# Kernel optimization log

Hardware: AMD Instinct MI355X
Metric: run time of the kernel (lower is better)

Reference implementation:

```python
import jax, jax.numpy as jnp
import numpy as np

B, D_IN, D_DENSE, S1, S2 = 16384, 1024, 1024, 1024, 1024
SPARSITY1, SPARSITY2 = 0.1, 0.01  # fraction of zeros in the 'sparse' weights


def setup_inputs() -> dict:
    key = jax.random.key(0)
    kx, k0, k1, k2, km1, km2 = jax.random.split(key, 6)
    x = jax.random.normal(kx, (B, D_IN), dtype=jnp.float32)
    # dense layer params (nn.Linear): weight [out, in], bias [out]
    w0 = jax.random.normal(k0, (D_DENSE, D_IN), dtype=jnp.float32) / np.sqrt(D_IN)
    b0 = jnp.zeros((D_DENSE,), dtype=jnp.float32)
    # sparse layers: dense randn weight elementwise-masked (mask keeps with prob 1-sparsity)
    w1 = jax.random.normal(k1, (S1, D_DENSE), dtype=jnp.float32)
    mask1 = jax.random.uniform(km1, (S1, D_DENSE)) > SPARSITY1
    b1 = jnp.zeros((S1,), dtype=jnp.float32)
    w2 = jax.random.normal(k2, (S2, S1), dtype=jnp.float32)
    mask2 = jax.random.uniform(km2, (S2, S1)) > SPARSITY2
    b2 = jnp.zeros((S2,), dtype=jnp.float32)
    return {"x": x, "w0": w0, "b0": b0, "w1": w1, "b1": b1, "mask1": mask1,
            "w2": w2, "b2": b2, "mask2": mask2}


def reference(x, w0, b0, w1, b1, mask1, w2, b2, mask2):
    # layer 1: dense linear + ReLU
    h = jax.nn.relu(jnp.einsum('bi,oi->bo', x, w0) + b0)
    # layer 2: masked ('sparse' COO in torch) linear + bias + ReLU
    h = jax.nn.relu(jnp.einsum('bi,oi->bo', h, w1 * mask1) + b1)
    # layer 3: masked linear + bias + ReLU
    out = jax.nn.relu(jnp.einsum('bi,oi->bo', h, w2 * mask2) + b2)
    return out
```

## Files before the change

### kernel.cpp

```cpp
#include <hip/hip_runtime.h>
#include <hip/hip_bf16.h>
#include <cstdint>
#include <cstddef>


typedef __bf16 bf16x8 __attribute__((ext_vector_type(8)));
typedef float  f32x4  __attribute__((ext_vector_type(4)));

#define AS1 __attribute__((address_space(1)))
#define AS3 __attribute__((address_space(3)))

__device__ __forceinline__ void gload_lds16(const void* g, void* l) {
    __builtin_amdgcn_global_load_lds((const AS1 void*)g, (AS3 void*)l, 16, 0, 0);
}

__global__ void detect_mask(const unsigned char* __restrict__ m, int* __restrict__ flag) {
    if (threadIdx.x != 0 || blockIdx.x != 0) return;
    int or1 = 0, or3 = 0;
    for (int e = 0; e < 256; ++e) { or1 |= m[e * 4 + 1]; or3 |= m[e * 4 + 3]; }
    *flag = or1 ? 1 : (or3 ? 2 : 0);
}

__global__ void cvt_bf16(const float* __restrict__ in, __bf16* __restrict__ out, long n) {
    long i = ((long)blockIdx.x * blockDim.x + threadIdx.x) * 8;
    if (i >= n) return;
    float4 a = *reinterpret_cast<const float4*>(in + i);
    float4 b = *reinterpret_cast<const float4*>(in + i + 4);
    bf16x8 o;
    o[0] = (__bf16)a.x; o[1] = (__bf16)a.y; o[2] = (__bf16)a.z; o[3] = (__bf16)a.w;
    o[4] = (__bf16)b.x; o[5] = (__bf16)b.y; o[6] = (__bf16)b.z; o[7] = (__bf16)b.w;
    *reinterpret_cast<bf16x8*>(out + i) = o;
}

__global__ void prep_w(const float* __restrict__ w, const void* __restrict__ mask,
                       const int* __restrict__ flag, __bf16* __restrict__ out, long n) {
    long i = ((long)blockIdx.x * blockDim.x + threadIdx.x) * 8;
    if (i >= n) return;
    float4 a = *reinterpret_cast<const float4*>(w + i);
    float4 b = *reinterpret_cast<const float4*>(w + i + 4);
    float v[8] = {a.x, a.y, a.z, a.w, b.x, b.y, b.z, b.w};
    if (mask) {
        const int mode = *flag;
        if (mode == 1) {
            const unsigned char* mp = (const unsigned char*)mask;
            #pragma unroll
            for (int j = 0; j < 8; ++j) v[j] = mp[i + j] ? v[j] : 0.f;
        } else if (mode == 0) {
            const int* mp = (const int*)mask;
            #pragma unroll
            for (int j = 0; j < 8; ++j) v[j] = mp[i + j] ? v[j] : 0.f;
        } else {
            const float* mp = (const float*)mask;
            #pragma unroll
            for (int j = 0; j < 8; ++j) v[j] = (mp[i + j] != 0.f) ? v[j] : 0.f;
        }
    }
    bf16x8 o;
    #pragma unroll
    for (int j = 0; j < 8; ++j) o[j] = (__bf16)v[j];
    *reinterpret_cast<bf16x8*>(out + i) = o;
}

__device__ __forceinline__ f32x4 mfma16(bf16x8 a, bf16x8 b, f32x4 c) {
    return __builtin_amdgcn_mfma_f32_16x16x32_bf16(a, b, c, 0, 0, 0);
}

#define MFMAQ(Q, A00, A01, A10, A11)                                        \
    __builtin_amdgcn_s_setprio(1);                                          \
    _Pragma("unroll")                                                       \
    for (int n = 0; n < 4; ++n) {                                           \
        acc[2*(Q)][n]   = mfma16(A00, b[n][0], acc[2*(Q)][n]);              \
        acc[2*(Q)][n]   = mfma16(A01, b[n][1], acc[2*(Q)][n]);              \
        acc[2*(Q)+1][n] = mfma16(A10, b[n][0], acc[2*(Q)+1][n]);            \
        acc[2*(Q)+1][n] = mfma16(A11, b[n][1], acc[2*(Q)+1][n]);            \
    }                                                                       \
    __builtin_amdgcn_s_setprio(0);

#define BAR() __builtin_amdgcn_s_barrier(); __builtin_amdgcn_sched_barrier(0)

template<bool F32OUT>
__global__ __launch_bounds__(512, 2) void gemm8p(
    const __bf16* __restrict__ A, const __bf16* __restrict__ W,
    const float* __restrict__ bias,
    __bf16* __restrict__ outb, float* __restrict__ outf) {
    constexpr int NT = 16;
    extern __shared__ char smem[];

    const int t   = threadIdx.x;
    const int l   = t & 63, l15 = l & 15, lhi = l >> 4;
    const int w   = t >> 6, wr = w >> 2, wc = w & 3;

    const int bid = blockIdx.x;
    const int swz = (bid & 7) * 32 + (bid >> 3);
    const int bx = swz & 3, by = swz >> 2;
    const int brow = by * 256, bcol = bx * 256;

    const int srow = t >> 3;
    const int scol = (((t & 7) ^ ((t >> 3) & 7)) << 4) >> 1;
    const __bf16* gA = A + (size_t)(brow + srow) * 1024 + scol;
    const __bf16* gW = W + (size_t)(bcol + srow) * 1024 + scol;
    const int woff = (t & 448) * 16;

    char* const ldsA = smem;
    char* const ldsB = smem + 65536;

    auto stageA = [&](int d, int h, int k0) {
        const __bf16* g = gA + (size_t)h * 131072 + k0;
        char* p = ldsA + d * 32768 + h * 16384 + woff;
        gload_lds16(g, p);
        gload_lds16(g + 65536, p + 8192);
    };
    auto stageB = [&](int d, int h, int k0) {
        const __bf16* g = gW + (size_t)h * 131072 + k0;
        char* p = ldsB + d * 32768 + h * 16384 + woff;
        gload_lds16(g, p);
        gload_lds16(g + 65536, p + 8192);
    };

    const int xorm  = (l & 7) << 4;
    const int koff0 = (lhi * 16) ^ xorm;
    const int koff1 = (64 + lhi * 16) ^ xorm;
    char* const aBase = ldsA + wr * 16384 + l15 * 128;
    char* const bBase = ldsB + (wc >> 1) * 16384 + ((wc & 1) * 64 + l15) * 128;

    f32x4 acc[8][4] = {};

    stageA(0, 0, 0); stageA(0, 1, 0);
    stageB(0, 0, 0); stageB(0, 1, 0);
    stageB(1, 0, 64); stageB(1, 1, 64);
    asm volatile("s_waitcnt vmcnt(4)" ::: "memory");
    BAR();

    #pragma unroll 2
    for (int tt = 0; tt < NT; ++tt) {
        const int d  = tt & 1;
        const int k1 = (tt + 1) * 64, k2 = (tt + 2) * 64;
        char* const aB = aBase + d * 32768;
        char* const bB = bBase + d * 32768;

        bf16x8 b[4][2];
        #pragma unroll
        for (int n = 0; n < 4; ++n) {
            b[n][0] = *(const bf16x8*)(bB + n * 2048 + koff0);
            b[n][1] = *(const bf16x8*)(bB + n * 2048 + koff1);
        }
        bf16x8 a00 = *(const bf16x8*)(aB + 0 * 2048 + koff0);
        bf16x8 a01 = *(const bf16x8*)(aB + 0 * 2048 + koff1);
        bf16x8 a10 = *(const bf16x8*)(aB + 1 * 2048 + koff0);
        bf16x8 a11 = *(const bf16x8*)(aB + 1 * 2048 + koff1);
        if (tt + 1 < NT) stageA(d ^ 1, 0, k1);
        MFMAQ(0, a00, a01, a10, a11);
        BAR();

        a00 = *(const bf16x8*)(aB + 2 * 2048 + koff0);
        a01 = *(const bf16x8*)(aB + 2 * 2048 + koff1);
        a10 = *(const bf16x8*)(aB + 3 * 2048 + koff0);
        a11 = *(const bf16x8*)(aB + 3 * 2048 + koff1);
        if (tt + 1 < NT) stageA(d ^ 1, 1, k1);
        if (tt + 2 < NT) stageB(d, 0, k2);
        MFMAQ(1, a00, a01, a10, a11);
        BAR();

        a00 = *(const bf16x8*)(aB + 4 * 2048 + koff0);
        a01 = *(const bf16x8*)(aB + 4 * 2048 + koff1);
        a10 = *(const bf16x8*)(aB + 5 * 2048 + koff0);
        a11 = *(const bf16x8*)(aB + 5 * 2048 + koff1);
        if (tt + 2 < NT) stageB(d, 1, k2);
        MFMAQ(2, a00, a01, a10, a11);
        BAR();

        a00 = *(const bf16x8*)(aB + 6 * 2048 + koff0);
        a01 = *(const bf16x8*)(aB + 6 * 2048 + koff1);
        a10 = *(const bf16x8*)(aB + 7 * 2048 + koff0);
        a11 = *(const bf16x8*)(aB + 7 * 2048 + koff1);
        MFMAQ(3, a00, a01, a10, a11);
        if (tt < NT - 1) {
            if (tt <= NT - 3) { asm volatile("s_waitcnt vmcnt(4)" ::: "memory"); }
            else              { asm volatile("s_waitcnt vmcnt(0)" ::: "memory"); }
            BAR();
        }
    }

    const int orow = brow + wr * 128 + lhi * 4;
    const int ocol = bcol + wc * 64 + l15;
    #pragma unroll
    for (int n = 0; n < 4; ++n) {
        const int col = ocol + n * 16;
        const float bv = bias[col];
        #pragma unroll
        for (int m = 0; m < 8; ++m) {
            const int r0 = orow + m * 16;
            #pragma unroll
            for (int r = 0; r < 4; ++r) {
                float v = acc[m][n][r] + bv;
                v = v > 0.f ? v : 0.f;
                if constexpr (F32OUT) outf[(size_t)(r0 + r) * 1024 + col] = v;
                else                  outb[(size_t)(r0 + r) * 1024 + col] = (__bf16)v;
            }
        }
    }
}

extern "C" void kernel_launch(void* const* d_in, const int* in_sizes, int n_in,
                              void* d_out, int out_size, void* d_ws, size_t ws_size,
                              hipStream_t stream) {
    const float* x  = (const float*)d_in[0];
    const float* w0 = (const float*)d_in[1];
    const float* b0 = (const float*)d_in[2];
    const float* w1 = (const float*)d_in[3];
    const float* b1 = (const float*)d_in[4];
    const void*  m1 = d_in[5];
    const float* w2 = (const float*)d_in[6];
    const float* b2 = (const float*)d_in[7];
    const void*  m2 = d_in[8];
    float* out = (float*)d_out;

    char* ws = (char*)d_ws;
    __bf16* xb  = (__bf16*)(ws);
    __bf16* h1  = (__bf16*)(ws + (size_t)32 * 1024 * 1024);
    __bf16* w0b = (__bf16*)(ws + (size_t)64 * 1024 * 1024);
    __bf16* w1b = w0b + 1024 * 1024;
    __bf16* w2b = w1b + 1024 * 1024;
    int*   flag = (int*)(w2b + 1024 * 1024);

    hipFuncSetAttribute((const void*)gemm8p<false>,
                        hipFuncAttributeMaxDynamicSharedMemorySize, 131072);
    hipFuncSetAttribute((const void*)gemm8p<true>,
                        hipFuncAttributeMaxDynamicSharedMemorySize, 131072);

    detect_mask<<<1, 64, 0, stream>>>((const unsigned char*)m1, flag);
    cvt_bf16<<<8192, 256, 0, stream>>>(x, xb, 16384L * 1024);
    prep_w<<<512, 256, 0, stream>>>(w0, nullptr, flag, w0b, 1024L * 1024);
    prep_w<<<512, 256, 0, stream>>>(w1, m1,      flag, w1b, 1024L * 1024);
    prep_w<<<512, 256, 0, stream>>>(w2, m2,      flag, w2b, 1024L * 1024);

    gemm8p<false><<<256, 512, 131072, stream>>>(xb, w0b, b0, h1, nullptr);
    gemm8p<false><<<256, 512, 131072, stream>>>(h1, w1b, b1, xb, nullptr);
    gemm8p<true ><<<256, 512, 131072, stream>>>(xb, w2b, b2, nullptr, out);
}
```

Measured before the change: 135.7 us.

## Merge prep kernels, restructure GEMM staging, and stage bf16 epilogue through LDS

Merges the x conversion and the three weight-prep launches into one kernel, and turns the single-thread mask detection into a wave ballot. In the GEMM main loop, the whole A tile is loaded in one step after the third quarter. The B-tile LDS layout changes, and the next quarter's A fragments are prefetched into registers before each MFMA batch, with explicit lgkmcnt waits. The bf16 epilogue writes through XOR-swizzled LDS so global stores are coalesced 16-byte vectors instead of scattered 2-byte stores. These target launch overhead, pipeline bubbles and uncoalesced output writes, at the cost of extra LDS synchronisation and more register pressure.

```diff
diff --git a/kernel.cpp b/kernel.cpp
--- a/kernel.cpp
+++ b/kernel.cpp
@@ -15,32 +15,21 @@
 }
 
 __global__ void detect_mask(const unsigned char* __restrict__ m, int* __restrict__ flag) {
-    if (threadIdx.x != 0 || blockIdx.x != 0) return;
+    const int t = threadIdx.x;
     int or1 = 0, or3 = 0;
-    for (int e = 0; e < 256; ++e) { or1 |= m[e * 4 + 1]; or3 |= m[e * 4 + 3]; }
-    *flag = or1 ? 1 : (or3 ? 2 : 0);
-}
-
-__global__ void cvt_bf16(const float* __restrict__ in, __bf16* __restrict__ out, long n) {
-    long i = ((long)blockIdx.x * blockDim.x + threadIdx.x) * 8;
-    if (i >= n) return;
-    float4 a = *reinterpret_cast<const float4*>(in + i);
-    float4 b = *reinterpret_cast<const float4*>(in + i + 4);
-    bf16x8 o;
-    o[0] = (__bf16)a.x; o[1] = (__bf16)a.y; o[2] = (__bf16)a.z; o[3] = (__bf16)a.w;
-    o[4] = (__bf16)b.x; o[5] = (__bf16)b.y; o[6] = (__bf16)b.z; o[7] = (__bf16)b.w;
-    *reinterpret_cast<bf16x8*>(out + i) = o;
-}
-
-__global__ void prep_w(const float* __restrict__ w, const void* __restrict__ mask,
-                       const int* __restrict__ flag, __bf16* __restrict__ out, long n) {
-    long i = ((long)blockIdx.x * blockDim.x + threadIdx.x) * 8;
-    if (i >= n) return;
+    for (int e = t; e < 256; e += 64) { or1 |= m[e * 4 + 1]; or3 |= m[e * 4 + 3]; }
+    unsigned long long b1 = __ballot(or1 != 0);
+    unsigned long long b3 = __ballot(or3 != 0);
+    if (t == 0) *flag = b1 ? 1 : (b3 ? 2 : 0);
+}
+
+__device__ __forceinline__ void prep_body(const float* __restrict__ w,
+                                          const void* __restrict__ mask, int mode,
+                                          __bf16* __restrict__ out, long i) {
     float4 a = *reinterpret_cast<const float4*>(w + i);
     float4 b = *reinterpret_cast<const float4*>(w + i + 4);
     float v[8] = {a.x, a.y, a.z, a.w, b.x, b.y, b.z, b.w};
     if (mask) {
-        const int mode = *flag;
         if (mode == 1) {
             const unsigned char* mp = (const unsigned char*)mask;
             #pragma unroll
@@ -59,6 +48,32 @@
     #pragma unroll
     for (int j = 0; j < 8; ++j) o[j] = (__bf16)v[j];
     *reinterpret_cast<bf16x8*>(out + i) = o;
+}
+
+__global__ void prep_all(const float* __restrict__ x, __bf16* __restrict__ xb,
+                         const float* __restrict__ w0, const float* __restrict__ w1,
+                         const float* __restrict__ w2,
+                         const void* __restrict__ m1, const void* __restrict__ m2,
+                         const int* __restrict__ flag,
+                         __bf16* __restrict__ w0b, __bf16* __restrict__ w1b,
+                         __bf16* __restrict__ w2b) {
+    const int bid = blockIdx.x;
+    if (bid < 8192) {
+        long i = ((long)bid * blockDim.x + threadIdx.x) * 8;
+        float4 a = *reinterpret_cast<const float4*>(x + i);
+        float4 b = *reinterpret_cast<const float4*>(x + i + 4);
+        bf16x8 o;
+        o[0] = (__bf16)a.x; o[1] = (__bf16)a.y; o[2] = (__bf16)a.z; o[3] = (__bf16)a.w;
+        o[4] = (__bf16)b.x; o[5] = (__bf16)b.y; o[6] = (__bf16)b.z; o[7] = (__bf16)b.w;
+        *reinterpret_cast<bf16x8*>(xb + i) = o;
+    } else {
+        const int q = bid - 8192, wi = q >> 9, sub = q & 511;
+        long i = ((long)sub * blockDim.x + threadIdx.x) * 8;
+        const int mode = *flag;
+        if (wi == 0)      prep_body(w0, nullptr, mode, w0b, i);
+        else if (wi == 1) prep_body(w1, m1,      mode, w1b, i);
+        else              prep_body(w2, m2,      mode, w2b, i);
+    }
 }
 
 __device__ __forceinline__ f32x4 mfma16(bf16x8 a, bf16x8 b, f32x4 c) {
@@ -76,7 +91,10 @@
     }                                                                       \
     __builtin_amdgcn_s_setprio(0);
 
-#define BAR() __builtin_amdgcn_s_barrier(); __builtin_amdgcn_sched_barrier(0)
+#define BAR()   __builtin_amdgcn_s_barrier(); __builtin_amdgcn_sched_barrier(0)
+#define LGKM0() asm volatile("s_waitcnt lgkmcnt(0)" ::: "memory")
+#define VM8()   asm volatile("s_waitcnt vmcnt(8)" ::: "memory")
+#define VM0()   asm volatile("s_waitcnt vmcnt(0)" ::: "memory")
 
 template<bool F32OUT>
 __global__ __launch_bounds__(512, 2) void gemm8p(
@@ -104,13 +122,15 @@
     char* const ldsA = smem;
     char* const ldsB = smem + 65536;
 
-    auto stageA = [&](int d, int h, int k0) {
-        const __bf16* g = gA + (size_t)h * 131072 + k0;
-        char* p = ldsA + d * 32768 + h * 16384 + woff;
-        gload_lds16(g, p);
-        gload_lds16(g + 65536, p + 8192);
+    auto stageAfull = [&](int d, int k0) {
+        const __bf16* g = gA + k0;
+        char* p = ldsA + d * 32768 + woff;
+        gload_lds16(g,          p);
+        gload_lds16(g + 65536,  p + 8192);
+        gload_lds16(g + 131072, p + 16384);
+        gload_lds16(g + 196608, p + 24576);
     };
-    auto stageB = [&](int d, int h, int k0) {
+    auto stageBh = [&](int d, int h, int k0) {
         const __bf16* g = gW + (size_t)h * 131072 + k0;
         char* p = ldsB + d * 32768 + h * 16384 + woff;
         gload_lds16(g, p);
@@ -121,22 +141,21 @@
     const int koff0 = (lhi * 16) ^ xorm;
     const int koff1 = (64 + lhi * 16) ^ xorm;
     char* const aBase = ldsA + wr * 16384 + l15 * 128;
-    char* const bBase = ldsB + (wc >> 1) * 16384 + ((wc & 1) * 64 + l15) * 128;
+    char* const bBase = ldsB + wc * 8192 + l15 * 128;
 
     f32x4 acc[8][4] = {};
 
-    stageA(0, 0, 0); stageA(0, 1, 0);
-    stageB(0, 0, 0); stageB(0, 1, 0);
-    stageB(1, 0, 64); stageB(1, 1, 64);
-    asm volatile("s_waitcnt vmcnt(4)" ::: "memory");
-    BAR();
+    stageAfull(0, 0);  stageBh(0, 0, 0);  stageBh(0, 1, 0);
+    stageAfull(1, 64); stageBh(1, 0, 64); stageBh(1, 1, 64);
+    VM8(); BAR();
 
     #pragma unroll 2
     for (int tt = 0; tt < NT; ++tt) {
         const int d  = tt & 1;
-        const int k1 = (tt + 1) * 64, k2 = (tt + 2) * 64;
+        const int k2 = (tt + 2) * 64;
         char* const aB = aBase + d * 32768;
         char* const bB = bBase + d * 32768;
+        const bool st = (tt + 2 < NT);
 
         bf16x8 b[4][2];
         #pragma unroll
@@ -148,55 +167,78 @@
         bf16x8 a01 = *(const bf16x8*)(aB + 0 * 2048 + koff1);
         bf16x8 a10 = *(const bf16x8*)(aB + 1 * 2048 + koff0);
         bf16x8 a11 = *(const bf16x8*)(aB + 1 * 2048 + koff1);
-        if (tt + 1 < NT) stageA(d ^ 1, 0, k1);
+        bf16x8 c00 = *(const bf16x8*)(aB + 2 * 2048 + koff0);
+        bf16x8 c01 = *(const bf16x8*)(aB + 2 * 2048 + koff1);
+        bf16x8 c10 = *(const bf16x8*)(aB + 3 * 2048 + koff0);
+        bf16x8 c11 = *(const bf16x8*)(aB + 3 * 2048 + koff1);
         MFMAQ(0, a00, a01, a10, a11);
-        BAR();
-
-        a00 = *(const bf16x8*)(aB + 2 * 2048 + koff0);
-        a01 = *(const bf16x8*)(aB + 2 * 2048 + koff1);
-        a10 = *(const bf16x8*)(aB + 3 * 2048 + koff0);
-        a11 = *(const bf16x8*)(aB + 3 * 2048 + koff1);
-        if (tt + 1 < NT) stageA(d ^ 1, 1, k1);
-        if (tt + 2 < NT) stageB(d, 0, k2);
-        MFMAQ(1, a00, a01, a10, a11);
-        BAR();
-
+        LGKM0(); BAR();
+
+        if (st) stageBh(d, 0, k2);
         a00 = *(const bf16x8*)(aB + 4 * 2048 + koff0);
         a01 = *(const bf16x8*)(aB + 4 * 2048 + koff1);
         a10 = *(const bf16x8*)(aB + 5 * 2048 + koff0);
         a11 = *(const bf16x8*)(aB + 5 * 2048 + koff1);
-        if (tt + 2 < NT) stageB(d, 1, k2);
+        MFMAQ(1, c00, c01, c10, c11);
+        LGKM0(); BAR();
+
+        if (st) stageBh(d, 1, k2);
+        c00 = *(const bf16x8*)(aB + 6 * 2048 + koff0);
+        c01 = *(const bf16x8*)(aB + 6 * 2048 + koff1);
+        c10 = *(const bf16x8*)(aB + 7 * 2048 + koff0);
+        c11 = *(const bf16x8*)(aB + 7 * 2048 + koff1);
         MFMAQ(2, a00, a01, a10, a11);
-        BAR();
-
-        a00 = *(const bf16x8*)(aB + 6 * 2048 + koff0);
-        a01 = *(const bf16x8*)(aB + 6 * 2048 + koff1);
-        a10 = *(const bf16x8*)(aB + 7 * 2048 + koff0);
-        a11 = *(const bf16x8*)(aB + 7 * 2048 + koff1);
-        MFMAQ(3, a00, a01, a10, a11);
-        if (tt < NT - 1) {
-            if (tt <= NT - 3) { asm volatile("s_waitcnt vmcnt(4)" ::: "memory"); }
-            else              { asm volatile("s_waitcnt vmcnt(0)" ::: "memory"); }
-            BAR();
-        }
-    }
-
-    const int orow = brow + wr * 128 + lhi * 4;
-    const int ocol = bcol + wc * 64 + l15;
-    #pragma unroll
-    for (int n = 0; n < 4; ++n) {
-        const int col = ocol + n * 16;
-        const float bv = bias[col];
-        #pragma unroll
-        for (int m = 0; m < 8; ++m) {
-            const int r0 = orow + m * 16;
-            #pragma unroll
-            for (int r = 0; r < 4; ++r) {
-                float v = acc[m][n][r] + bv;
-                v = v > 0.f ? v : 0.f;
-                if constexpr (F32OUT) outf[(size_t)(r0 + r) * 1024 + col] = v;
-                else                  outb[(size_t)(r0 + r) * 1024 + col] = (__bf16)v;
+        LGKM0(); BAR();
+
+        if (st) stageAfull(d, k2);
+        MFMAQ(3, c00, c01, c10, c11);
+        if (tt <= NT - 3)      { VM8(); BAR(); }
+        else if (tt == NT - 2) { VM0(); BAR(); }
+    }
+
+    if constexpr (F32OUT) {
+        const int orow = brow + wr * 128 + lhi * 4;
+        const int ocol = bcol + wc * 64 + l15;
+        #pragma unroll
+        for (int n = 0; n < 4; ++n) {
+            const int col = ocol + n * 16;
+            const float bv = bias[col];
+            #pragma unroll
+            for (int m = 0; m < 8; ++m) {
+                const int r0 = orow + m * 16;
+                #pragma unroll
+                for (int r = 0; r < 4; ++r) {
+                    float v = acc[m][n][r] + bv;
+                    outf[(size_t)(r0 + r) * 1024 + col] = v > 0.f ? v : 0.f;
+                }
             }
+        }
+    } else {
+        __syncthreads();
+        char* const cl = smem;
+        #pragma unroll
+        for (int n = 0; n < 4; ++n) {
+            const int colb = (wc * 64 + n * 16 + l15) * 2;
+            const float bv = bias[bcol + wc * 64 + n * 16 + l15];
+            #pragma unroll
+            for (int m = 0; m < 8; ++m) {
+                #pragma unroll
+                for (int r = 0; r < 4; ++r) {
+                    const int row = wr * 128 + m * 16 + lhi * 4 + r;
+                    float v = acc[m][n][r] + bv;
+                    v = v > 0.f ? v : 0.f;
+                    *(__bf16*)(cl + row * 512 + (colb ^ ((row & 12) << 3))) = (__bf16)v;
+                }
+            }
+        }
+        __syncthreads();
+        #pragma unroll
+        for (int rd = 0; rd < 16; ++rd) {
+            const int off = rd * 8192 + t * 16;
+            const int row = off >> 9;
+            const int cb  = (off & 511) ^ ((row & 12) << 3);
+            bf16x8 v = *(const bf16x8*)(cl + off);
+            *(bf16x8*)((char*)outb + ((size_t)(brow + row) * 1024 + bcol) * 2 + cb) = v;
         }
     }
 }
@@ -229,10 +271,8 @@
                         hipFuncAttributeMaxDynamicSharedMemorySize, 131072);
 
     detect_mask<<<1, 64, 0, stream>>>((const unsigned char*)m1, flag);
-    cvt_bf16<<<8192, 256, 0, stream>>>(x, xb, 16384L * 1024);
-    prep_w<<<512, 256, 0, stream>>>(w0, nullptr, flag, w0b, 1024L * 1024);
-    prep_w<<<512, 256, 0, stream>>>(w1, m1,      flag, w1b, 1024L * 1024);
-    prep_w<<<512, 256, 0, stream>>>(w2, m2,      flag, w2b, 1024L * 1024);
+    prep_all<<<9728, 256, 0, stream>>>(x, xb, w0, w1, w2, m1, m2, flag,
+                                       w0b, w1b, w2b);
 
     gemm8p<false><<<256, 512, 131072, stream>>>(xb, w0b, b0, h1, nullptr);
     gemm8p<false><<<256, 512, 131072, stream>>>(h1, w1b, b1, xb, nullptr);
```

New measurement: 127.0 us. 6.5% less time.
